# Kernel tuning notes

Hardware: AMD Instinct MI355X
Metric: run time of the kernel (lower is better)

The kernel has to match this reference:

```python
import jax, jax.numpy as jnp
import numpy as np

D_MODEL = 2048
N_HEADS = 16
N_KV_HEADS = 4
D_K = D_MODEL // N_HEADS  # 128
N_REP = N_HEADS // N_KV_HEADS
WINDOW = 128  # current_window_size default
RMS_EPS = 1e-8
ROPE_BASE = 10000.0
MASK_FILL = -10000.0


def _rmsnorm(x, w):
    rms = jnp.sqrt(jnp.mean(x * x, axis=-1, keepdims=True) + RMS_EPS)
    return x / rms * w


def _rope(x, cos, sin):
    # x: [B, S, H, d_k]; cos/sin: [S, d_k//2]; pairs are interleaved (..., -1, 2)
    B, S, H, dk = x.shape
    xr = x.reshape(B, S, H, dk // 2, 2)
    x1, x2 = xr[..., 0], xr[..., 1]
    c = cos[None, :, None, :]
    s = sin[None, :, None, :]
    o1 = x1 * c - x2 * s
    o2 = x1 * s + x2 * c
    return jnp.stack([o1, o2], axis=-1).reshape(B, S, H, dk)


def setup_inputs() -> dict:
    key = jax.random.key(0)
    ks = jax.random.split(key, 10)
    B, S = 2, 2048
    std = 1.0 / np.sqrt(D_MODEL)
    inp = {
        "x": jax.random.normal(ks[0], (B, S, D_MODEL), dtype=jnp.float32),
        "Wq": jax.random.normal(ks[1], (D_MODEL, D_MODEL), dtype=jnp.float32) * std,
        "bq": jnp.zeros((D_MODEL,), dtype=jnp.float32),
        "Wk": jax.random.normal(ks[2], (N_KV_HEADS * D_K, D_MODEL), dtype=jnp.float32) * std,
        "bk": jnp.zeros((N_KV_HEADS * D_K,), dtype=jnp.float32),
        "Wv": jax.random.normal(ks[3], (N_KV_HEADS * D_K, D_MODEL), dtype=jnp.float32) * std,
        "bv": jnp.zeros((N_KV_HEADS * D_K,), dtype=jnp.float32),
        "Wo": jax.random.normal(ks[4], (D_MODEL, D_MODEL), dtype=jnp.float32) * std,
        "bo": jnp.zeros((D_MODEL,), dtype=jnp.float32),
        "qn_w": jnp.ones((D_K,), dtype=jnp.float32),
        "kn_w": jnp.ones((D_K,), dtype=jnp.float32),
        "scale": jnp.asarray(1.0 / np.sqrt(D_K), dtype=jnp.float32),
    }
    return inp


def reference(x, Wq, bq, Wk, bk, Wv, bv, Wo, bo, qn_w, kn_w, scale):
    B, S, D = x.shape
    # projections
    q = (x @ Wq.T + bq).reshape(B, S, N_HEADS, D_K)
    k = (x @ Wk.T + bk).reshape(B, S, N_KV_HEADS, D_K)
    v = (x @ Wv.T + bv).reshape(B, S, N_KV_HEADS, D_K)
    # per-head RMSNorm
    q = _rmsnorm(q, qn_w)
    k = _rmsnorm(k, kn_w)
    # RoPE
    inv_freq = 1.0 / (ROPE_BASE ** (jnp.arange(0, D_K, 2, dtype=jnp.float32) / D_K))
    t = jnp.arange(S, dtype=jnp.float32)
    freqs = t[:, None] * inv_freq[None, :]  # [S, D_K//2]
    cos, sin = jnp.cos(freqs), jnp.sin(freqs)
    q = _rope(q, cos, sin)
    k = _rope(k, cos, sin)
    # [B, H, S, d_k]
    q = q.transpose(0, 2, 1, 3)
    k = k.transpose(0, 2, 1, 3)
    v = v.transpose(0, 2, 1, 3)
    # GQA repeat (repeat_interleave on head dim)
    k = jnp.repeat(k, N_REP, axis=1)
    v = jnp.repeat(v, N_REP, axis=1)
    # dense sliding-window path (window < seq_len)
    scores = jnp.einsum("bhqd,bhkd->bhqk", q, k) * scale
    idx = jnp.arange(S)
    causal = idx[:, None] < idx[None, :]  # triu diag=1
    local = jnp.abs(idx[:, None] - idx[None, :]) > (WINDOW // 2)
    mask = causal | local
    scores = jnp.where(mask[None, None, :, :], MASK_FILL, scores)
    attn = jax.nn.softmax(scores, axis=-1)
    out = jnp.einsum("bhqk,bhkd->bhqd", attn, v)
    out = out.transpose(0, 2, 1, 3).reshape(B, S, D)
    return out @ Wo.T + bo
```

## Files before the change

kernel.cpp:

```cpp
#include <hip/hip_runtime.h>

#define BATCH 2
#define SEQ 2048
#define DMODEL 2048
#define NHEADS 16
#define NKV 4
#define DK 128
#define WINH 64
#define NQKV 3072

typedef unsigned short ushort_t;
typedef __attribute__((ext_vector_type(8))) __bf16 bf16x8;
typedef __attribute__((ext_vector_type(4))) float f32x4;

__device__ __forceinline__ float b2f(ushort_t u) {
    union { unsigned int i; float f; } v; v.i = ((unsigned int)u) << 16; return v.f;
}
__device__ __forceinline__ ushort_t f2b(float f) {
    union { float f; unsigned int i; } v; v.f = f;
    unsigned int r = v.i + 0x7FFFu + ((v.i >> 16) & 1u);
    return (ushort_t)(r >> 16);
}

__device__ __forceinline__ void gload_lds16(const ushort_t* g, ushort_t* l) {
    __builtin_amdgcn_global_load_lds(
        (__attribute__((address_space(1))) void*)(void*)const_cast<ushort_t*>(g),
        (__attribute__((address_space(3))) void*)l, 16, 0, 0);
}

__global__ __launch_bounds__(256) void prep(
    const float* __restrict__ x,  const float* __restrict__ Wq,
    const float* __restrict__ Wk, const float* __restrict__ Wv,
    const float* __restrict__ Wo, const float* __restrict__ bq,
    const float* __restrict__ bk, const float* __restrict__ bv,
    ushort_t* __restrict__ xb, ushort_t* __restrict__ wdst,
    float* __restrict__ bqkv, float2* __restrict__ rtab)
{
    const int blk = blockIdx.x;
    const int tid = threadIdx.x;
    if (blk < 4096) {
        int i = blk * 256 + tid;
        float4 a = *((const float4*)x + i * 2);
        float4 b = *((const float4*)x + i * 2 + 1);
        ushort_t o[8] = { f2b(a.x), f2b(a.y), f2b(a.z), f2b(a.w),
                          f2b(b.x), f2b(b.y), f2b(b.z), f2b(b.w) };
        *((uint4*)xb + i) = *(const uint4*)o;
    } else if (blk < 9216) {
        int i = (blk - 4096) * 256 + tid;
        int row = i >> 8, c8 = i & 255;
        const float* src;
        if      (row < 2048) src = Wq + (size_t)row * 2048;
        else if (row < 2560) src = Wk + (size_t)(row - 2048) * 2048;
        else if (row < 3072) src = Wv + (size_t)(row - 2560) * 2048;
        else                 src = Wo + (size_t)(row - 3072) * 2048;
        float4 a = *((const float4*)src + c8 * 2);
        float4 b = *((const float4*)src + c8 * 2 + 1);
        ushort_t o[8] = { f2b(a.x), f2b(a.y), f2b(a.z), f2b(a.w),
                          f2b(b.x), f2b(b.y), f2b(b.z), f2b(b.w) };
        *((uint4*)wdst + i) = *(const uint4*)o;
    } else if (blk < 9228) {
        int i = (blk - 9216) * 256 + tid;
        if (i < 2048) bqkv[i] = bq[i];
        else if (i < 2560) bqkv[i] = bk[i - 2048];
        else if (i < 3072) bqkv[i] = bv[i - 2560];
    } else {
        int i = (blk - 9228) * 256 + tid;
        int s = i >> 6, dd = i & 63;
        float invfreq = exp2f(-(float)(2 * dd) * (13.287712379549449f / 128.0f));
        float ang = (float)s * invfreq;
        rtab[i] = make_float2(cosf(ang), sinf(ang));
    }
}

__global__ __launch_bounds__(512) void gemm_qkv_p(
    const ushort_t* __restrict__ A, const ushort_t* __restrict__ W,
    const float* __restrict__ bias, ushort_t* __restrict__ C,
    int M, int N, int K)
{
    extern __shared__ __attribute__((aligned(16))) ushort_t smem[];

    const int tid  = threadIdx.x;
    const int lane = tid & 63;
    const int wave = tid >> 6;
    const int wm   = wave >> 2;
    const int wn   = wave & 3;
    const int nbn  = N / 192;

    int nwg = gridDim.x;
    int bid = blockIdx.x;
    int nb  = (nwg & 7) ? bid : ((bid & 7) * (nwg >> 3) + (bid >> 3));
    const int bm = nb / nbn;
    const int bn = nb % nbn;
    const int m0 = bm << 8;
    const int n0 = bn * 192;

    f32x4 acc[8][3] = {};

    const int frow = lane & 15;
    const int kg   = lane >> 4;

    const ushort_t* gA[4]; const ushort_t* gB[3];
    int aofs[4], bofs[3];
#pragma unroll
    for (int j = 0; j < 4; ++j) {
        int c = j * 512 + tid;
        int r = c >> 3, s = c & 7;
        gA[j] = A + (size_t)(m0 + r) * K + (s ^ (r & 7)) * 8;
        aofs[j] = (j * 512 + wave * 64) * 8;
    }
#pragma unroll
    for (int j = 0; j < 3; ++j) {
        int c = j * 512 + tid;
        int r = c >> 3, s = c & 7;
        gB[j] = W + (size_t)(n0 + r) * K + (s ^ (r & 7)) * 8;
        bofs[j] = (j * 512 + wave * 64) * 8;
    }

    const int nt = K >> 6;
#pragma unroll
    for (int j = 0; j < 4; ++j) gload_lds16(gA[j], smem + aofs[j]);
#pragma unroll
    for (int j = 0; j < 3; ++j) gload_lds16(gB[j], smem + 32768 + bofs[j]);

    for (int t = 0; t < nt; ++t) {
        const int cur = t & 1;
        if (t + 1 < nt) {
            const int nxt = cur ^ 1;
            const int ko = (t + 1) << 6;
#pragma unroll
            for (int j = 0; j < 4; ++j)
                gload_lds16(gA[j] + ko, smem + nxt * 16384 + aofs[j]);
#pragma unroll
            for (int j = 0; j < 3; ++j)
                gload_lds16(gB[j] + ko, smem + 32768 + nxt * 12288 + bofs[j]);
            asm volatile("s_waitcnt vmcnt(7)" ::: "memory");
        } else {
            asm volatile("s_waitcnt vmcnt(0)" ::: "memory");
        }
        __builtin_amdgcn_s_barrier();
        __builtin_amdgcn_sched_barrier(0);

        const ushort_t* bufA = smem + cur * 16384;
        const ushort_t* bufB = smem + 32768 + cur * 12288;
#pragma unroll
        for (int kk = 0; kk < 2; ++kk) {
            bf16x8 af[8], bf[3];
#pragma unroll
            for (int mf = 0; mf < 8; ++mf) {
                int r = wm * 128 + mf * 16 + frow;
                af[mf] = *(const bf16x8*)(bufA + (r * 8 + ((kk * 4 + kg) ^ (r & 7))) * 8);
            }
#pragma unroll
            for (int nf = 0; nf < 3; ++nf) {
                int r = wn * 48 + nf * 16 + frow;
                bf[nf] = *(const bf16x8*)(bufB + (r * 8 + ((kk * 4 + kg) ^ (r & 7))) * 8);
            }
#pragma unroll
            for (int mf = 0; mf < 8; ++mf)
#pragma unroll
                for (int nf = 0; nf < 3; ++nf)
                    acc[mf][nf] = __builtin_amdgcn_mfma_f32_16x16x32_bf16(
                        af[mf], bf[nf], acc[mf][nf], 0, 0, 0);
        }
        asm volatile("s_waitcnt lgkmcnt(0)" ::: "memory");
        __builtin_amdgcn_s_barrier();
        __builtin_amdgcn_sched_barrier(0);
    }

    const int orow = (lane >> 4) << 2;
    const int ocol = lane & 15;
#pragma unroll
    for (int nf = 0; nf < 3; ++nf) {
        int col = n0 + wn * 48 + nf * 16 + ocol;
        float bvf = bias[col];
#pragma unroll
        for (int mf = 0; mf < 8; ++mf) {
#pragma unroll
            for (int r = 0; r < 4; ++r) {
                int row = m0 + wm * 128 + mf * 16 + orow + r;
                C[(size_t)row * N + col] = f2b(acc[mf][nf][r] + bvf);
            }
        }
    }
}

__global__ __launch_bounds__(512) void gemm_out_ks(
    const ushort_t* __restrict__ A, const ushort_t* __restrict__ W,
    const float* __restrict__ bias, float* __restrict__ C,
    int M, int N, int K)
{
    __shared__ __attribute__((aligned(16))) unsigned char smem[65536];
    float* red = (float*)smem;

    const int tid  = threadIdx.x;
    const int lane = tid & 63;
    const int wave = tid >> 6;
    const int g    = wave >> 2;
    const int q    = wave & 3;
    const int wm   = q >> 1, wn = q & 1;
    const int nbn  = N >> 7;

    int nwg = gridDim.x;
    int bid = blockIdx.x;
    int nb  = (nwg & 7) ? bid : ((bid & 7) * (nwg >> 3) + (bid >> 3));
    const int bm = nb / nbn;
    const int bn = nb % nbn;
    const int m0 = bm << 7, n0 = bn << 7;

    f32x4 acc[4][4] = {};

    const int frow = lane & 15;
    const int kg   = lane >> 4;

    const ushort_t* gA[2]; const ushort_t* gB[2];
    int eofs[2];
#pragma unroll
    for (int j = 0; j < 2; ++j) {
        int t = wave * 2 + j;
        int c = t * 64 + lane;
        int r = c >> 3, s = c & 7;
        int ksrc = s ^ (r & 7);
        gA[j] = A + (size_t)(m0 + r) * K + ksrc * 8;
        gB[j] = W + (size_t)(n0 + r) * K + ksrc * 8;
        eofs[j] = t * 512;
    }

    const int nt = K >> 6;
#pragma unroll
    for (int j = 0; j < 2; ++j) {
        gload_lds16(gA[j], (ushort_t*)smem + eofs[j]);
        gload_lds16(gB[j], (ushort_t*)(smem + 16384) + eofs[j]);
    }
    __syncthreads();

    for (int t = 0; t < nt; ++t) {
        const int cur = t & 1;
        if (t + 1 < nt) {
            const int nxt = cur ^ 1;
            const int ko = (t + 1) << 6;
#pragma unroll
            for (int j = 0; j < 2; ++j) {
                gload_lds16(gA[j] + ko, (ushort_t*)(smem + nxt * 32768) + eofs[j]);
                gload_lds16(gB[j] + ko, (ushort_t*)(smem + nxt * 32768 + 16384) + eofs[j]);
            }
        }
        const ushort_t* bufA = (const ushort_t*)(smem + cur * 32768);
        const ushort_t* bufB = (const ushort_t*)(smem + cur * 32768 + 16384);

        bf16x8 af[4], bfr[4];
#pragma unroll
        for (int mi = 0; mi < 4; ++mi) {
            int r = (wm << 6) + (mi << 4) + frow;
            int sl = ((g << 2) + kg) ^ (r & 7);
            af[mi] = *(const bf16x8*)(bufA + (r * 8 + sl) * 8);
        }
#pragma unroll
        for (int ni = 0; ni < 4; ++ni) {
            int r = (wn << 6) + (ni << 4) + frow;
            int sl = ((g << 2) + kg) ^ (r & 7);
            bfr[ni] = *(const bf16x8*)(bufB + (r * 8 + sl) * 8);
        }
#pragma unroll
        for (int mi = 0; mi < 4; ++mi)
#pragma unroll
            for (int ni = 0; ni < 4; ++ni)
                acc[mi][ni] = __builtin_amdgcn_mfma_f32_16x16x32_bf16(
                    af[mi], bfr[ni], acc[mi][ni], 0, 0, 0);

        __syncthreads();
    }

    if (g == 1) {
#pragma unroll
        for (int mi = 0; mi < 4; ++mi)
#pragma unroll
            for (int ni = 0; ni < 4; ++ni)
                *(f32x4*)(red + q * 4096 + (mi * 4 + ni) * 256 + lane * 4) =
                    acc[mi][ni];
    }
    __syncthreads();

    if (g == 0) {
        const int orow = (lane >> 4) << 2;
        const int ocol = lane & 15;
#pragma unroll
        for (int ni = 0; ni < 4; ++ni) {
            int col = n0 + (wn << 6) + (ni << 4) + ocol;
            float bvf = bias[col];
#pragma unroll
            for (int mi = 0; mi < 4; ++mi) {
                f32x4 other = *(const f32x4*)(red + q * 4096 + (mi * 4 + ni) * 256 + lane * 4);
#pragma unroll
                for (int r = 0; r < 4; ++r) {
                    int row = m0 + (wm << 6) + (mi << 4) + orow + r;
                    C[(size_t)row * N + col] = acc[mi][ni][r] + other[r] + bvf;
                }
            }
        }
    }
}

__global__ __launch_bounds__(256) void attn_mfma(
    const ushort_t* __restrict__ qkv, const float* __restrict__ qn_w,
    const float* __restrict__ kn_w, const float* __restrict__ scp,
    const float2* __restrict__ rtab, ushort_t* __restrict__ ao)
{
    __shared__ __attribute__((aligned(16))) ushort_t sK[16384];
    __shared__ __attribute__((aligned(16))) ushort_t sVT[16384];

    const int tid  = threadIdx.x;
    const int lane = tid & 63;
    const int w    = tid >> 6;
    const int c    = lane & 15;
    const int g    = lane >> 4;

    const int blk = blockIdx.x;
    const int qt  = blk & 31;
    const int h   = (blk >> 5) & 15;
    const int b   = blk >> 9;
    const int kvh = h >> 2;
    const int i0  = qt << 6;
    const int jb  = i0 - 64;
    const float scale = scp[0];

    bf16x8 aq[4];
    {
        const int srow = i0 + w * 16 + c;
        const ushort_t* qp = qkv + ((size_t)(b * 2048 + srow)) * NQKV
                                 + h * 128 + g * 8;
        float xv[4][8];
        float ss = 0.f;
#pragma unroll
        for (int ks = 0; ks < 4; ++ks) {
            ushort_t raw[8];
            *(uint4*)raw = *(const uint4*)(qp + ks * 32);
#pragma unroll
            for (int j = 0; j < 8; ++j) {
                float xf = b2f(raw[j]);
                xv[ks][j] = xf;
                ss += xf * xf;
            }
        }
        ss += __shfl_xor(ss, 16, 64);
        ss += __shfl_xor(ss, 32, 64);
        float inv = rsqrtf(ss * (1.0f / 128.0f) + 1e-8f) * scale;
#pragma unroll
        for (int ks = 0; ks < 4; ++ks) {
            ushort_t outb[8];
#pragma unroll
            for (int jj = 0; jj < 4; ++jj) {
                int d = ks * 32 + g * 8 + 2 * jj;
                float2 w2 = *(const float2*)(qn_w + d);
                float x0 = xv[ks][2 * jj]     * inv * w2.x;
                float x1 = xv[ks][2 * jj + 1] * inv * w2.y;
                float2 cs = rtab[(srow << 6) + (d >> 1)];
                outb[2 * jj]     = f2b(x0 * cs.x - x1 * cs.y);
                outb[2 * jj + 1] = f2b(x0 * cs.y + x1 * cs.x);
            }
            aq[ks] = *(const bf16x8*)outb;
        }
    }

    const ushort_t* kvb = qkv + ((size_t)b * 2048) * NQKV + 2048 + kvh * 128;
#pragma unroll
    for (int it = 0; it < 8; ++it) {
        int idx = it * 256 + tid;
        int rr = idx >> 4, cc = idx & 15;
        int j = jb + rr; if (j < 0) j = 0;
        ushort_t raw[8];
        *(uint4*)raw = *(const uint4*)(kvb + (size_t)j * NQKV + cc * 8);
        float xv[8];
        float ss = 0.f;
#pragma unroll
        for (int jj = 0; jj < 8; ++jj) {
            xv[jj] = b2f(raw[jj]);
            ss += xv[jj] * xv[jj];
        }
        ss += __shfl_xor(ss, 1, 64);
        ss += __shfl_xor(ss, 2, 64);
        ss += __shfl_xor(ss, 4, 64);
        ss += __shfl_xor(ss, 8, 64);
        float inv = rsqrtf(ss * (1.0f / 128.0f) + 1e-8f);
        ushort_t outb[8];
#pragma unroll
        for (int jj = 0; jj < 4; ++jj) {
            int d = cc * 8 + 2 * jj;
            float2 w2 = *(const float2*)(kn_w + d);
            float x0 = xv[2 * jj]     * inv * w2.x;
            float x1 = xv[2 * jj + 1] * inv * w2.y;
            float2 cs = rtab[(j << 6) + (d >> 1)];
            outb[2 * jj]     = f2b(x0 * cs.x - x1 * cs.y);
            outb[2 * jj + 1] = f2b(x0 * cs.y + x1 * cs.x);
        }
        int f2v = (rr & 15) ^ ((rr >> 3) & 15);
        *(uint4*)(sK + (rr * 16 + (cc ^ f2v)) * 8) = *(const uint4*)outb;
    }
#pragma unroll
    for (int it = 0; it < 4; ++it) {
        int task = it * 256 + tid;
        int pp = task >> 4, d8 = task & 15;
        int j0 = jb + 2 * pp;     if (j0 < 0) j0 = 0;
        int j1 = jb + 2 * pp + 1; if (j1 < 0) j1 = 0;
        ushort_t e0[8]; *(uint4*)e0 = *(const uint4*)(kvb + (size_t)j0 * NQKV + 512 + d8 * 8);
        ushort_t e1[8]; *(uint4*)e1 = *(const uint4*)(kvb + (size_t)j1 * NQKV + 512 + d8 * 8);
        int cc = pp >> 2;
#pragma unroll
        for (int jj = 0; jj < 8; ++jj) {
            int rr = d8 * 8 + jj;
            int f2v = (rr & 15) ^ ((rr >> 3) & 15);
            unsigned int word = (unsigned int)e0[jj] | ((unsigned int)e1[jj] << 16);
            *(unsigned int*)(sVT + (rr * 16 + (cc ^ f2v)) * 8 + (pp & 3) * 2) = word;
        }
    }
    __syncthreads();

    f32x4 s[8] = {};
#pragma unroll
    for (int nt = 0; nt < 8; ++nt) {
        int rr = nt * 16 + c;
        int f2v = (rr & 15) ^ ((rr >> 3) & 15);
#pragma unroll
        for (int ks = 0; ks < 4; ++ks) {
            bf16x8 bk = *(const bf16x8*)(sK + (rr * 16 + ((ks * 4 + g) ^ f2v)) * 8);
            s[nt] = __builtin_amdgcn_mfma_f32_16x16x32_bf16(aq[ks], bk, s[nt], 0, 0, 0);
        }
    }

    float linv[4];
#pragma unroll
    for (int r = 0; r < 4; ++r) {
        int qb = w * 16 + g * 4 + r;
#pragma unroll
        for (int nt = 0; nt < 8; ++nt) {
            int jl = nt * 16 + c;
            bool valid = (jl >= qb) && (jl <= qb + 64) && (i0 + jl >= 64);
            s[nt][r] = valid ? s[nt][r] : -1e30f;
        }
        float m = s[0][r];
#pragma unroll
        for (int nt = 1; nt < 8; ++nt) m = fmaxf(m, s[nt][r]);
#pragma unroll
        for (int off = 1; off <= 8; off <<= 1) m = fmaxf(m, __shfl_xor(m, off, 64));
        float sum = 0.f;
#pragma unroll
        for (int nt = 0; nt < 8; ++nt) {
            float e = __expf(s[nt][r] - m);
            s[nt][r] = e;
            sum += e;
        }
#pragma unroll
        for (int off = 1; off <= 8; off <<= 1) sum += __shfl_xor(sum, off, 64);
        linv[r] = 1.0f / sum;
    }

    __syncthreads();
    float* Pw = (float*)sK + w * 2048;
#pragma unroll
    for (int nt = 0; nt < 8; ++nt) {
#pragma unroll
        for (int r = 0; r < 4; ++r) {
            int q = g * 4 + r;
            int chunk = nt * 4 + (c >> 2);
            Pw[q * 128 + ((chunk ^ (q & 7)) * 4) + (c & 3)] = s[nt][r];
        }
    }

    f32x4 o[8] = {};
#pragma unroll
    for (int kt = 0; kt < 4; ++kt) {
        float pf[8];
#pragma unroll
        for (int e = 0; e < 2; ++e) {
            int chunk = kt * 8 + g * 2 + e;
            f32x4 v4 = *(const f32x4*)(Pw + c * 128 + ((chunk ^ (c & 7)) * 4));
            pf[e * 4 + 0] = v4[0]; pf[e * 4 + 1] = v4[1];
            pf[e * 4 + 2] = v4[2]; pf[e * 4 + 3] = v4[3];
        }
        ushort_t pb[8];
#pragma unroll
        for (int j = 0; j < 8; ++j) pb[j] = f2b(pf[j]);
        bf16x8 pa = *(const bf16x8*)pb;
#pragma unroll
        for (int dt = 0; dt < 8; ++dt) {
            int rr = dt * 16 + c;
            int f2v = (rr & 15) ^ ((rr >> 3) & 15);
            bf16x8 bv = *(const bf16x8*)(sVT + (rr * 16 + ((kt * 4 + g) ^ f2v)) * 8);
            o[dt] = __builtin_amdgcn_mfma_f32_16x16x32_bf16(pa, bv, o[dt], 0, 0, 0);
        }
    }

    const size_t orow0 = (size_t)(b * 2048 + i0 + w * 16);
#pragma unroll
    for (int dt = 0; dt < 8; ++dt) {
#pragma unroll
        for (int r = 0; r < 4; ++r) {
            int q = g * 4 + r;
            ao[(orow0 + q) * 2048 + h * 128 + dt * 16 + c] = f2b(o[dt][r] * linv[r]);
        }
    }
}

extern "C" void kernel_launch(void* const* d_in, const int* in_sizes, int n_in,
                              void* d_out, int out_size, void* d_ws, size_t ws_size,
                              hipStream_t stream)
{
    const float* x   = (const float*)d_in[0];
    const float* Wq  = (const float*)d_in[1];
    const float* bq  = (const float*)d_in[2];
    const float* Wk  = (const float*)d_in[3];
    const float* bk  = (const float*)d_in[4];
    const float* Wv  = (const float*)d_in[5];
    const float* bv  = (const float*)d_in[6];
    const float* Wo  = (const float*)d_in[7];
    const float* bo  = (const float*)d_in[8];
    const float* qnw = (const float*)d_in[9];
    const float* knw = (const float*)d_in[10];
    const float* scp = (const float*)d_in[11];
    float* out = (float*)d_out;

    const int M = BATCH * SEQ;
    ushort_t* xb    = (ushort_t*)d_ws;
    ushort_t* qkv0  = xb   + (size_t)M * DMODEL;
    ushort_t* Wqkvb = qkv0 + (size_t)M * NQKV;
    ushort_t* Wob   = Wqkvb + (size_t)NQKV * DMODEL;
    float*    bqkv  = (float*)(Wob + (size_t)DMODEL * DMODEL);
    float2*   rtab  = (float2*)(bqkv + 3072);
    ushort_t* ao    = xb;
    (void)ws_size; (void)in_sizes; (void)n_in; (void)out_size;

    hipFuncSetAttribute((const void*)gemm_qkv_p,
                        hipFuncAttributeMaxDynamicSharedMemorySize, 114688);

    prep<<<dim3(9740), 256, 0, stream>>>(x, Wq, Wk, Wv, Wo, bq, bk, bv,
                                         xb, Wqkvb, bqkv, rtab);
    gemm_qkv_p<<<dim3((M / 256) * (NQKV / 192)), 512, 114688, stream>>>(
        xb, Wqkvb, bqkv, qkv0, M, NQKV, DMODEL);
    attn_mfma<<<dim3(BATCH * NHEADS * (SEQ / 64)), 256, 0, stream>>>(
        qkv0, qnw, knw, scp, rtab, ao);
    gemm_out_ks<<<dim3((M / 128) * (DMODEL / 128)), 512, 0, stream>>>(
        ao, Wob, bo, out, M, DMODEL, DMODEL);
}
```

Baseline: 136.3 us.

## Restructure QKV GEMM into 256x256 tiles with 8-stage half-tile LDS pipeline

The QKV projection GEMM moves from 256x192 tiles with double buffering to 256x256 tiles. Each K step is split into 32-wide A and B half-stages held in an 8-slot LDS ring, with loads issued 6 stages ahead and finer-grained waits. MFMA sections in the GEMM and the attention kernel are wrapped in s_setprio so waves in their matrix phase get issue priority. The goal is deeper overlap of global-to-LDS loads with compute and more reuse per tile. The cost is more LDS (128KB), more barriers per K step, and fewer workgroups (192 instead of 256), which may hurt load balance across CUs.

```diff
diff --git a/kernel.cpp b/kernel.cpp
--- a/kernel.cpp
+++ b/kernel.cpp
@@ -72,7 +72,7 @@
     }
 }
 
-__global__ __launch_bounds__(512) void gemm_qkv_p(
+__global__ __launch_bounds__(512) void gemm_qkv_8p(
     const ushort_t* __restrict__ A, const ushort_t* __restrict__ W,
     const float* __restrict__ bias, ushort_t* __restrict__ C,
     int M, int N, int K)
@@ -84,100 +84,105 @@
     const int wave = tid >> 6;
     const int wm   = wave >> 2;
     const int wn   = wave & 3;
-    const int nbn  = N / 192;
+    const int nbn  = N >> 8;
 
     int nwg = gridDim.x;
     int bid = blockIdx.x;
     int nb  = (nwg & 7) ? bid : ((bid & 7) * (nwg >> 3) + (bid >> 3));
     const int bm = nb / nbn;
     const int bn = nb % nbn;
-    const int m0 = bm << 8;
-    const int n0 = bn * 192;
-
-    f32x4 acc[8][3] = {};
+    const int m0 = bm << 8, n0 = bn << 8;
+
+    f32x4 acc[8][4] = {};
 
     const int frow = lane & 15;
     const int kg   = lane >> 4;
 
-    const ushort_t* gA[4]; const ushort_t* gB[3];
-    int aofs[4], bofs[3];
-#pragma unroll
-    for (int j = 0; j < 4; ++j) {
-        int c = j * 512 + tid;
-        int r = c >> 3, s = c & 7;
-        gA[j] = A + (size_t)(m0 + r) * K + (s ^ (r & 7)) * 8;
-        aofs[j] = (j * 512 + wave * 64) * 8;
-    }
-#pragma unroll
-    for (int j = 0; j < 3; ++j) {
-        int c = j * 512 + tid;
-        int r = c >> 3, s = c & 7;
-        gB[j] = W + (size_t)(n0 + r) * K + (s ^ (r & 7)) * 8;
-        bofs[j] = (j * 512 + wave * 64) * 8;
+    const ushort_t* aP[2]; const ushort_t* bP[2]; int lofs[2];
+#pragma unroll
+    for (int rd = 0; rd < 2; ++rd) {
+        int c = rd * 512 + tid;
+        int r = c >> 2, s = c & 3;
+        int ks = s ^ ((r >> 1) & 3);
+        aP[rd] = A + (size_t)(m0 + r) * K + ks * 8;
+        bP[rd] = W + (size_t)(n0 + r) * K + ks * 8;
+        lofs[rd] = (rd * 512 + wave * 64) * 8;
     }
 
     const int nt = K >> 6;
-#pragma unroll
-    for (int j = 0; j < 4; ++j) gload_lds16(gA[j], smem + aofs[j]);
-#pragma unroll
-    for (int j = 0; j < 3; ++j) gload_lds16(gB[j], smem + 32768 + bofs[j]);
+    const int H  = nt << 2;
+
+    auto stage = [&](int h) {
+        int ts = h >> 2, j = h & 3;
+        int kofs = (ts << 6) + ((j >> 1) << 5);
+        ushort_t* dst = smem + (h & 7) * 8192;
+        if ((j & 1) == 0) {
+            gload_lds16(aP[0] + kofs, dst + lofs[0]);
+            gload_lds16(aP[1] + kofs, dst + lofs[1]);
+        } else {
+            gload_lds16(bP[0] + kofs, dst + lofs[0]);
+            gload_lds16(bP[1] + kofs, dst + lofs[1]);
+        }
+    };
+
+#pragma unroll
+    for (int h = 0; h < 6; ++h) stage(h);
 
     for (int t = 0; t < nt; ++t) {
-        const int cur = t & 1;
-        if (t + 1 < nt) {
-            const int nxt = cur ^ 1;
-            const int ko = (t + 1) << 6;
-#pragma unroll
-            for (int j = 0; j < 4; ++j)
-                gload_lds16(gA[j] + ko, smem + nxt * 16384 + aofs[j]);
-#pragma unroll
-            for (int j = 0; j < 3; ++j)
-                gload_lds16(gB[j] + ko, smem + 32768 + nxt * 12288 + bofs[j]);
-            asm volatile("s_waitcnt vmcnt(7)" ::: "memory");
-        } else {
-            asm volatile("s_waitcnt vmcnt(0)" ::: "memory");
-        }
-        __builtin_amdgcn_s_barrier();
-        __builtin_amdgcn_sched_barrier(0);
-
-        const ushort_t* bufA = smem + cur * 16384;
-        const ushort_t* bufB = smem + 32768 + cur * 12288;
-#pragma unroll
-        for (int kk = 0; kk < 2; ++kk) {
-            bf16x8 af[8], bf[3];
-#pragma unroll
-            for (int mf = 0; mf < 8; ++mf) {
-                int r = wm * 128 + mf * 16 + frow;
-                af[mf] = *(const bf16x8*)(bufA + (r * 8 + ((kk * 4 + kg) ^ (r & 7))) * 8);
-            }
-#pragma unroll
-            for (int nf = 0; nf < 3; ++nf) {
-                int r = wn * 48 + nf * 16 + frow;
-                bf[nf] = *(const bf16x8*)(bufB + (r * 8 + ((kk * 4 + kg) ^ (r & 7))) * 8);
-            }
-#pragma unroll
-            for (int mf = 0; mf < 8; ++mf)
-#pragma unroll
-                for (int nf = 0; nf < 3; ++nf)
-                    acc[mf][nf] = __builtin_amdgcn_mfma_f32_16x16x32_bf16(
-                        af[mf], bf[nf], acc[mf][nf], 0, 0, 0);
-        }
-        asm volatile("s_waitcnt lgkmcnt(0)" ::: "memory");
-        __builtin_amdgcn_s_barrier();
-        __builtin_amdgcn_sched_barrier(0);
+#pragma unroll
+        for (int q = 0; q < 4; ++q) {
+            const int p = (t << 2) + q;
+            if (p + 6 < H) stage(p + 6);
+            if (q == 0) {
+                if (t == nt - 1) asm volatile("s_waitcnt vmcnt(4)" ::: "memory");
+                else             asm volatile("s_waitcnt vmcnt(8)" ::: "memory");
+            } else if (q == 2) {
+                if (t == nt - 1) asm volatile("s_waitcnt vmcnt(0)" ::: "memory");
+                else             asm volatile("s_waitcnt vmcnt(8)" ::: "memory");
+            }
+            __builtin_amdgcn_s_barrier();
+            asm volatile("" ::: "memory");
+            __builtin_amdgcn_sched_barrier(0);
+
+            const int kk = q >> 1, mh = q & 1;
+            const ushort_t* As = smem + (((t << 2) + (kk << 1)) & 7) * 8192;
+            const ushort_t* Bs = smem + (((t << 2) + (kk << 1) + 1) & 7) * 8192;
+            bf16x8 af[4], bf[4];
+#pragma unroll
+            for (int mf = 0; mf < 4; ++mf) {
+                int r = (wm << 7) + ((mh << 2) + mf) * 16 + frow;
+                af[mf] = *(const bf16x8*)(As + (r * 4 + (kg ^ ((r >> 1) & 3))) * 8);
+            }
+#pragma unroll
+            for (int nf = 0; nf < 4; ++nf) {
+                int r = (wn << 6) + nf * 16 + frow;
+                bf[nf] = *(const bf16x8*)(Bs + (r * 4 + (kg ^ ((r >> 1) & 3))) * 8);
+            }
+            __builtin_amdgcn_s_setprio(1);
+#pragma unroll
+            for (int mf = 0; mf < 4; ++mf)
+#pragma unroll
+                for (int nf = 0; nf < 4; ++nf)
+                    acc[(mh << 2) + mf][nf] = __builtin_amdgcn_mfma_f32_16x16x32_bf16(
+                        af[mf], bf[nf], acc[(mh << 2) + mf][nf], 0, 0, 0);
+            __builtin_amdgcn_s_setprio(0);
+            asm volatile("s_waitcnt lgkmcnt(0)" ::: "memory");
+            __builtin_amdgcn_s_barrier();
+            __builtin_amdgcn_sched_barrier(0);
+        }
     }
 
     const int orow = (lane >> 4) << 2;
     const int ocol = lane & 15;
 #pragma unroll
-    for (int nf = 0; nf < 3; ++nf) {
-        int col = n0 + wn * 48 + nf * 16 + ocol;
+    for (int nf = 0; nf < 4; ++nf) {
+        int col = n0 + (wn << 6) + nf * 16 + ocol;
         float bvf = bias[col];
 #pragma unroll
         for (int mf = 0; mf < 8; ++mf) {
 #pragma unroll
             for (int r = 0; r < 4; ++r) {
-                int row = m0 + wm * 128 + mf * 16 + orow + r;
+                int row = m0 + (wm << 7) + mf * 16 + orow + r;
                 C[(size_t)row * N + col] = f2b(acc[mf][nf][r] + bvf);
             }
         }
@@ -415,6 +420,7 @@
     __syncthreads();
 
     f32x4 s[8] = {};
+    __builtin_amdgcn_s_setprio(1);
 #pragma unroll
     for (int nt = 0; nt < 8; ++nt) {
         int rr = nt * 16 + c;
@@ -425,6 +431,7 @@
             s[nt] = __builtin_amdgcn_mfma_f32_16x16x32_bf16(aq[ks], bk, s[nt], 0, 0, 0);
         }
     }
+    __builtin_amdgcn_s_setprio(0);
 
     float linv[4];
 #pragma unroll
@@ -480,6 +487,7 @@
 #pragma unroll
         for (int j = 0; j < 8; ++j) pb[j] = f2b(pf[j]);
         bf16x8 pa = *(const bf16x8*)pb;
+        __builtin_amdgcn_s_setprio(1);
 #pragma unroll
         for (int dt = 0; dt < 8; ++dt) {
             int rr = dt * 16 + c;
@@ -487,6 +495,7 @@
             bf16x8 bv = *(const bf16x8*)(sVT + (rr * 16 + ((kt * 4 + g) ^ f2v)) * 8);
             o[dt] = __builtin_amdgcn_mfma_f32_16x16x32_bf16(pa, bv, o[dt], 0, 0, 0);
         }
+        __builtin_amdgcn_s_setprio(0);
     }
 
     const size_t orow0 = (size_t)(b * 2048 + i0 + w * 16);
@@ -528,12 +537,12 @@
     ushort_t* ao    = xb;
     (void)ws_size; (void)in_sizes; (void)n_in; (void)out_size;
 
-    hipFuncSetAttribute((const void*)gemm_qkv_p,
-                        hipFuncAttributeMaxDynamicSharedMemorySize, 114688);
+    hipFuncSetAttribute((const void*)gemm_qkv_8p,
+                        hipFuncAttributeMaxDynamicSharedMemorySize, 131072);
 
     prep<<<dim3(9740), 256, 0, stream>>>(x, Wq, Wk, Wv, Wo, bq, bk, bv,
                                          xb, Wqkvb, bqkv, rtab);
-    gemm_qkv_p<<<dim3((M / 256) * (NQKV / 192)), 512, 114688, stream>>>(
+    gemm_qkv_8p<<<dim3((M / 256) * (NQKV / 256)), 512, 131072, stream>>>(
         xb, Wqkvb, bqkv, qkv0, M, NQKV, DMODEL);
     attn_mfma<<<dim3(BATCH * NHEADS * (SEQ / 64)), 256, 0, stream>>>(
         qkv0, qnw, knw, scp, rtab, ao);
```

After: 148.5 us. 8.9% more time.
